# Optimization experiments

Measured on AMD Instinct MI355X. Metric: run time of the kernel, lower is better.

The kernel has to match this reference:

```python
import jax, jax.numpy as jnp
from jax import lax
import numpy as np

EMBED, HIDDEN, VOCAB = 512, 512, 10000
ATT, ENC = 512, 2048
B, NPIX, T = 128, 49, 30


def _lin(k, out_d, in_d):
    k1, k2 = jax.random.split(k)
    s = 1.0 / np.sqrt(in_d)
    return (jax.random.uniform(k1, (out_d, in_d), minval=-s, maxval=s),
            jax.random.uniform(k2, (out_d,), minval=-s, maxval=s))


def setup_inputs() -> dict:
    key = jax.random.key(0)
    ks = jax.random.split(key, 24)
    inp = {}
    inp['enc_image'] = jax.random.normal(ks[0], (B, NPIX, ENC))
    inp['global_features'] = jax.random.normal(ks[1], (B, ENC))
    inp['encoded_captions'] = jax.random.randint(ks[2], (B, T), 0, VOCAB)
    lens = jax.random.randint(ks[3], (B,), 1, T + 1).at[0].set(T)
    inp['caption_lengths'] = lens[:, None]
    # parameters
    inp['emb_W'] = jax.random.uniform(ks[4], (VOCAB, EMBED), minval=-0.1, maxval=0.1)
    inp['e2h_W'], inp['e2h_b'] = _lin(ks[5], HIDDEN, ENC)
    inp['gf_W'], inp['gf_b'] = _lin(ks[6], EMBED, ENC)
    inp['fc_W'] = jax.random.uniform(ks[7], (VOCAB, HIDDEN), minval=-0.1, maxval=0.1)
    inp['fc_b'] = jnp.zeros((VOCAB,))
    inp['lstm_Wih'], inp['lstm_bih'] = _lin(ks[8], 4 * HIDDEN, 2 * EMBED)
    inp['lstm_Whh'], inp['lstm_bhh'] = _lin(ks[9], 4 * HIDDEN, HIDDEN)
    inp['xg_W'], inp['xg_b'] = _lin(ks[10], HIDDEN, 2 * EMBED)
    inp['hg_W'], inp['hg_b'] = _lin(ks[11], HIDDEN, HIDDEN)
    inp['senaff_W'], inp['senaff_b'] = _lin(ks[12], HIDDEN, HIDDEN)
    inp['senatt_W'], inp['senatt_b'] = _lin(ks[13], ATT, HIDDEN)
    inp['haff_W'], inp['haff_b'] = _lin(ks[14], HIDDEN, HIDDEN)
    inp['hatt_W'], inp['hatt_b'] = _lin(ks[15], ATT, HIDDEN)
    inp['vatt_W'], inp['vatt_b'] = _lin(ks[16], ATT, HIDDEN)
    inp['alph_W'], inp['alph_b'] = _lin(ks[17], 1, ATT)
    inp['ctx_W'], inp['ctx_b'] = _lin(ks[18], HIDDEN, HIDDEN)
    return inp


def reference(enc_image, global_features, encoded_captions, caption_lengths,
              emb_W, e2h_W, e2h_b, gf_W, gf_b, fc_W, fc_b,
              lstm_Wih, lstm_bih, lstm_Whh, lstm_bhh,
              xg_W, xg_b, hg_W, hg_b,
              senaff_W, senaff_b, senatt_W, senatt_b,
              haff_W, haff_b, hatt_W, hatt_b,
              vatt_W, vatt_b, alph_W, alph_b, ctx_W, ctx_b):
    lengths = caption_lengths[:, 0]
    order = jnp.argsort(-lengths)                     # descending (stable)
    lengths = lengths[order]
    spatial = jax.nn.relu(jnp.einsum('bpe,he->bph', enc_image[order], e2h_W) + e2h_b)  # (B,NP,H)
    gimg = jax.nn.relu(global_features[order] @ gf_W.T + gf_b)                          # (B,E)
    embs = emb_W[encoded_captions[order]]                                               # (B,T,E)
    inputs = jnp.concatenate([embs, jnp.broadcast_to(gimg[:, None, :], embs.shape)], axis=-1)  # (B,T,2E)
    vattn = jnp.einsum('bph,ah->bpa', spatial, vatt_W) + vatt_b                         # (B,NP,A) hoisted
    h0 = jnp.zeros((spatial.shape[0], HIDDEN), spatial.dtype)
    c0 = h0

    def step(carry, xs):
        h, c = carry
        xt, mask = xs                                  # (B,2E), (B,) bool = row still active
        gates = xt @ lstm_Wih.T + lstm_bih + h @ lstm_Whh.T + lstm_bhh
        i, f, g, o = jnp.split(gates, 4, axis=-1)
        c_new = jax.nn.sigmoid(f) * c + jax.nn.sigmoid(i) * jnp.tanh(g)
        h_new = jax.nn.sigmoid(o) * jnp.tanh(c_new)
        st = jax.nn.sigmoid(xt @ xg_W.T + xg_b + h @ hg_W.T + hg_b) * jnp.tanh(c_new)  # sentinel
        sen_aff = jax.nn.relu(st @ senaff_W.T + senaff_b)    # (B,H)
        sen_att = sen_aff @ senatt_W.T + senatt_b            # (B,A)
        h_aff = jnp.tanh(h_new @ haff_W.T + haff_b)
        h_att = h_aff @ hatt_W.T + hatt_b
        att_feats = jnp.concatenate([vattn, sen_att[:, None, :]], axis=1)   # (B,NP+1,A)
        scores = jnp.tanh(att_feats + h_att[:, None, :]) @ alph_W[0] + alph_b[0]
        alpha = jax.nn.softmax(scores, axis=1)               # (B,NP+1)
        cat_feats = jnp.concatenate([spatial, sen_aff[:, None, :]], axis=1)
        context = jnp.einsum('bph,bp->bh', cat_feats, alpha)
        out_l = jnp.tanh((context + h_aff) @ ctx_W.T + ctx_b)
        pt = out_l @ fc_W.T + fc_b                           # dropout = identity (eval)
        m = mask[:, None]
        return (jnp.where(m, h_new, h), jnp.where(m, c_new, c)), jnp.where(m, pt, 0.0)

    masks = lengths[None, :] > jnp.arange(T)[:, None]        # (T,B) replicates shrinking batch_size_t
    _, preds = lax.scan(step, (h0, c0), (jnp.swapaxes(inputs, 0, 1), masks))
    return jnp.swapaxes(preds, 0, 1)                         # (B,T,VOCAB), sorted-by-length order
```

## Files before the change

kernel.cpp:

```cpp
#include <hip/hip_runtime.h>
#include <hip/hip_bf16.h>
#include <cstdint>
#include <cstddef>

#define DEVI __device__ __forceinline__

#define BB 128
#define TT 30
#define VOCAB 10000
#define ENCD 2048
#define NPIX 49
#define SLOT 65536

typedef __attribute__((ext_vector_type(8))) short bf16x8;
typedef __attribute__((ext_vector_type(4))) float f32x4;

DEVI float bf2f(unsigned short u){ union{float f; unsigned int i;} x; x.i=((unsigned)u)<<16; return x.f; }
DEVI unsigned short f2bf(float f){ union{float f; unsigned int i;} x; x.f=f; unsigned r=x.i + 0x7fffu + ((x.i>>16)&1u); return (unsigned short)(r>>16); }
DEVI float sigm(float x){ return 1.0f/(1.0f+expf(-x)); }
DEVI f32x4 mfma16(bf16x8 a, bf16x8 b, f32x4 c){ return __builtin_amdgcn_mfma_f32_16x16x32_bf16(a,b,c,0,0,0); }

DEVI uint4 byp16(const void* p){
  const unsigned long long* q=(const unsigned long long*)p;
  unsigned long long a=__hip_atomic_load(q,   __ATOMIC_RELAXED, __HIP_MEMORY_SCOPE_AGENT);
  unsigned long long b=__hip_atomic_load(q+1, __ATOMIC_RELAXED, __HIP_MEMORY_SCOPE_AGENT);
  uint4 r; r.x=(unsigned)a; r.y=(unsigned)(a>>32); r.z=(unsigned)b; r.w=(unsigned)(b>>32); return r;
}
DEVI unsigned byp4(const void* p){
  return __hip_atomic_load((const unsigned*)p, __ATOMIC_RELAXED, __HIP_MEMORY_SCOPE_AGENT);
}
DEVI void byps4(unsigned short* p, unsigned v){
  __hip_atomic_store((unsigned*)p, v, __ATOMIC_RELAXED, __HIP_MEMORY_SCOPE_AGENT);
}

DEVI void waitarr(int* base, int n, int thresh){
  __syncthreads();
  if(threadIdx.x < 64){
    for(;;){
      int v = (threadIdx.x<n) ? __hip_atomic_load(base + threadIdx.x*16, __ATOMIC_RELAXED, __HIP_MEMORY_SCOPE_AGENT)
                              : 0x7fffffff;
      if(__all(v >= thresh)) break;
      __builtin_amdgcn_s_sleep(8);
    }
  }
  asm volatile("" ::: "memory");
  __syncthreads();
}
DEVI void setflag(int* f, int val){
  __syncthreads();
  if(threadIdx.x==0) __hip_atomic_store(f, val, __ATOMIC_RELAXED, __HIP_MEMORY_SCOPE_AGENT);
}

__global__ void k_sort(const int* __restrict__ lens, int* __restrict__ order, int* __restrict__ Bt){
  __shared__ int L[BB];
  int i = threadIdx.x;
  L[i] = lens[i];
  __syncthreads();
  int li = L[i]; int rank = 0;
  for(int j=0;j<BB;j++){ int lj=L[j]; rank += (lj>li) || (lj==li && j<i); }
  order[rank] = i;
  if(i<TT){ int c=0; for(int j=0;j<BB;j++) c += (L[j]>i); Bt[i]=c; }
}

struct WC13 { const float* src[13]; unsigned short* dst[13]; int n[13]; };
__global__ void k_wconv(WC13 wc){
  int stride = gridDim.x*blockDim.x;
  int tid0 = blockIdx.x*blockDim.x + threadIdx.x;
  for(int s=0;s<13;s++){
    const float4* src=(const float4*)wc.src[s];
    int n4 = wc.n[s]>>2;
    ushort4* dst=(ushort4*)wc.dst[s];
    for(int i=tid0;i<n4;i+=stride){
      float4 v=src[i];
      ushort4 o; o.x=f2bf(v.x); o.y=f2bf(v.y); o.z=f2bf(v.z); o.w=f2bf(v.w);
      dst[i]=o;
    }
  }
}

__global__ void k_xt(const int* __restrict__ caps, const int* __restrict__ order,
                     const float* __restrict__ embW, const unsigned short* __restrict__ gimg,
                     unsigned short* __restrict__ xt){
  int total=BB*TT*1024;
  for(int idx=blockIdx.x*blockDim.x+threadIdx.x; idx<total; idx+=gridDim.x*blockDim.x){
    int k=idx&1023; int bt=idx>>10; int t=bt%TT; int b=bt/TT;
    unsigned short v;
    if(k<512){ int tok=caps[order[b]*TT+t]; v=f2bf(embW[(size_t)tok*512+k]); }
    else v=gimg[b*512+(k-512)];
    xt[idx]=v;
  }
}

__global__ __launch_bounds__(256) void k_gemm_f32A2(
    const float* __restrict__ A, int lda, int rpb, const int* __restrict__ order,
    const unsigned short* __restrict__ W, const float* __restrict__ bias,
    unsigned short* __restrict__ out, int K)
{
  __shared__ unsigned short As[128][136];
  int tid=threadIdx.x, wave=tid>>6, lane=tid&63, l15=lane&15, l4=lane>>4;
  int mb = blockIdx.y*128;
  f32x4 acc[8][4];
  f32x4 z = {0.f,0.f,0.f,0.f};
  #pragma unroll
  for(int i=0;i<8;i++)
    #pragma unroll
    for(int j=0;j<4;j++) acc[i][j]=z;
  int cch=tid&15, r0=tid>>4;
  int nb = blockIdx.x*256 + wave*64;
  for(int kc=0;kc<K;kc+=128){
    __syncthreads();
    #pragma unroll
    for(int rp=0;rp<8;rp++){
      int r=r0+rp*16;
      int m=mb+r;
      int sb = order[m/rpb]*rpb + m%rpb;
      const float* p = A + (size_t)sb*lda + kc + cch*8;
      float4 v0=*(const float4*)p, v1=*(const float4*)(p+4);
      unsigned short* d=&As[r][cch*8];
      d[0]=f2bf(v0.x); d[1]=f2bf(v0.y); d[2]=f2bf(v0.z); d[3]=f2bf(v0.w);
      d[4]=f2bf(v1.x); d[5]=f2bf(v1.y); d[6]=f2bf(v1.z); d[7]=f2bf(v1.w);
    }
    __syncthreads();
    #pragma unroll
    for(int kk=0;kk<4;kk++){
      bf16x8 bfr[4];
      #pragma unroll
      for(int nt=0;nt<4;nt++)
        bfr[nt] = *(const bf16x8*)(W + (size_t)(nb+nt*16+l15)*K + kc + kk*32 + l4*8);
      #pragma unroll
      for(int mt=0;mt<8;mt++){
        bf16x8 af = *(const bf16x8*)&As[mt*16+l15][kk*32+l4*8];
        #pragma unroll
        for(int nt=0;nt<4;nt++) acc[mt][nt]=mfma16(af,bfr[nt],acc[mt][nt]);
      }
    }
  }
  #pragma unroll
  for(int nt=0;nt<4;nt++){
    int n = nb + nt*16 + l15;
    float bs = bias[n];
    #pragma unroll
    for(int mt=0;mt<8;mt++){
      #pragma unroll
      for(int j=0;j<4;j++){
        int row = mb + mt*16 + l4*4 + j;
        float v = acc[mt][nt][j]+bs; v = v>0.f ? v : 0.f;
        out[(size_t)row*512 + n] = f2bf(v);
      }
    }
  }
}

DEVI void dev_gemm512c(unsigned short (*As)[136], const unsigned short* A, const unsigned short* W,
                       const float* bias, unsigned short* out, int xtile){
  int tid=threadIdx.x, wave=tid>>6, lane=tid&63, l15=lane&15, l4=lane>>4;
  f32x4 acc[8];
  f32x4 z = {0.f,0.f,0.f,0.f};
  #pragma unroll
  for(int i=0;i<8;i++) acc[i]=z;
  int cch=tid&15, r0=tid>>4;
  int nrow = xtile*64 + wave*16 + l15;
  for(int kc=0;kc<512;kc+=128){
    __syncthreads();
    #pragma unroll
    for(int rp=0;rp<8;rp++){
      int r=r0+rp*16;
      *(uint4*)&As[r][cch*8] = *(const uint4*)(A + (size_t)r*512 + kc + cch*8);
    }
    __syncthreads();
    #pragma unroll
    for(int kk=0;kk<4;kk++){
      bf16x8 bfr = *(const bf16x8*)(W + (size_t)nrow*512 + kc + kk*32 + l4*8);
      #pragma unroll
      for(int mt=0;mt<8;mt++){
        bf16x8 af = *(const bf16x8*)&As[mt*16+l15][kk*32+l4*8];
        acc[mt]=mfma16(af,bfr,acc[mt]);
      }
    }
  }
  float bs = bias ? bias[nrow] : 0.f;
  #pragma unroll
  for(int mt=0;mt<8;mt++){
    #pragma unroll
    for(int j=0;j<4;j++){
      int row = mt*16 + l4*4 + j;
      out[(size_t)row*512+nrow]=f2bf(acc[mt][j]+bs);
    }
  }
  __syncthreads();
}

struct PreD { const unsigned short* A; const unsigned short* W; const float* bias; unsigned short* out; };
struct PreD2 { PreD d[2]; };
__global__ __launch_bounds__(256) void k_pre(PreD2 dd){
  __shared__ unsigned short As[128][136];
  PreD g = dd.d[blockIdx.z];
  dev_gemm512c(As, g.A + (size_t)blockIdx.y*128*512, g.W, g.bias,
               g.out + (size_t)blockIdx.y*128*512, blockIdx.x);
}

__global__ __launch_bounds__(256) void k_gx(
    const unsigned short* __restrict__ xt, const unsigned short* __restrict__ w_ih,
    const unsigned short* __restrict__ w_xg,
    const float* __restrict__ bih, const float* __restrict__ bhh,
    const float* __restrict__ bxg, const float* __restrict__ bhg,
    unsigned short* __restrict__ Gx)
{
  __shared__ unsigned short As[128][136];
  int tid=threadIdx.x, wave=tid>>6, lane=tid&63, l15=lane&15, l4=lane>>4;
  int t = blockIdx.y;
  f32x4 acc[8];
  f32x4 z = {0.f,0.f,0.f,0.f};
  #pragma unroll
  for(int i=0;i<8;i++) acc[i]=z;
  int cch=tid&15, r0=tid>>4;
  int n = blockIdx.x*64 + wave*16 + l15;
  const unsigned short* wrow = (n<2048) ? (w_ih + (size_t)n*1024) : (w_xg + (size_t)(n-2048)*1024);
  for(int kc=0;kc<1024;kc+=128){
    __syncthreads();
    #pragma unroll
    for(int rp=0;rp<8;rp++){
      int r=r0+rp*16;
      *(uint4*)&As[r][cch*8] = *(const uint4*)(xt + (size_t)r*(TT*1024) + t*1024 + kc + cch*8);
    }
    __syncthreads();
    #pragma unroll
    for(int kk=0;kk<4;kk++){
      bf16x8 bfr = *(const bf16x8*)(wrow + kc + kk*32 + l4*8);
      #pragma unroll
      for(int mt=0;mt<8;mt++){
        bf16x8 af = *(const bf16x8*)&As[mt*16+l15][kk*32+l4*8];
        acc[mt]=mfma16(af,bfr,acc[mt]);
      }
    }
  }
  float bias = (n<2048) ? (bih[n]+bhh[n]) : (bxg[n-2048]+bhg[n-2048]);
  #pragma unroll
  for(int mt=0;mt<8;mt++){
    int row = mt*16 + l4*4;
    ushort4 o;
    o.x=f2bf(acc[mt][0]+bias); o.y=f2bf(acc[mt][1]+bias);
    o.z=f2bf(acc[mt][2]+bias); o.w=f2bf(acc[mt][3]+bias);
    *(ushort4*)(Gx + ((size_t)t*2560 + n)*128 + row) = o;
  }
}

struct PCtx {
  const unsigned short *w_hh, *w_hg, *Gx;
  const unsigned short *w_saff, *w_satt, *w_haff, *w_hatt, *w_ctx, *w_fc;
  const unsigned short *vattn, *SC;
  const float *sab,*stbias,*hab,*htb, *alW,*alb, *cxb, *fcb;
  const int *Bt;
  unsigned short *h_hist;
  unsigned short *stb;
  unsigned short *sbuf;
  float *dout;
  int *Lf,*SAf,*SBf,*S3f;
};

DEVI void stage_full(unsigned short (*As2)[520], const unsigned short* src){
  int tid=threadIdx.x;
  #pragma unroll
  for(int i=0;i<32;i++){
    int idx = i*256 + tid;
    int r = idx>>6, c = (idx&63)<<3;
    *(uint4*)&As2[r][c] = byp16(src + (size_t)r*512 + c);
  }
}

DEVI void dev_lstm3(unsigned short (*As2)[520], const PCtx& p, int t, int cb,
                    const unsigned short* hprev, unsigned short* hout, float creg[2][4]){
  int tid=threadIdx.x, wave=tid>>6, lane=tid&63, l15=lane&15, l4=lane>>4;
  int jb = cb*16;
  __syncthreads();
  stage_full(As2, hprev);
  f32x4 acc[2][5];
  #pragma unroll
  for(int m=0;m<2;m++){
    #pragma unroll
    for(int s=0;s<5;s++){
      int col = (s<4) ? (s*512 + jb + l15) : (2048 + jb + l15);
      int row = (wave*2+m)*16 + l4*4;
      ushort4 g = *(const ushort4*)(p.Gx + ((size_t)t*2560 + col)*128 + row);
      acc[m][s][0]=bf2f(g.x); acc[m][s][1]=bf2f(g.y); acc[m][s][2]=bf2f(g.z); acc[m][s][3]=bf2f(g.w);
    }
  }
  __syncthreads();
  #pragma unroll
  for(int kk=0;kk<16;kk++){
    int kg = kk*32 + l4*8;
    bf16x8 bfr[5];
    #pragma unroll
    for(int s=0;s<5;s++){
      const unsigned short* wp = (s<4) ? (p.w_hh + (size_t)(s*512+jb+l15)*512 + kg)
                                       : (p.w_hg + (size_t)(jb+l15)*512 + kg);
      bfr[s] = *(const bf16x8*)wp;
    }
    #pragma unroll
    for(int m=0;m<2;m++){
      bf16x8 af = *(const bf16x8*)&As2[(wave*2+m)*16+l15][kk*32+l4*8];
      #pragma unroll
      for(int s=0;s<5;s++) acc[m][s]=mfma16(af,bfr[s],acc[m][s]);
    }
  }
  int bt = p.Bt[t];
  int j = jb + l15;
  unsigned short* stt = p.stb + (size_t)t*SLOT;
  #pragma unroll
  for(int m=0;m<2;m++){
    int mt = wave*2+m;
    #pragma unroll
    for(int jj=0;jj<4;jj++){
      int b = mt*16 + l4*4 + jj;
      float iv = sigm(acc[m][0][jj]);
      float fv = sigm(acc[m][1][jj]);
      float gv = tanhf(acc[m][2][jj]);
      float ov = sigm(acc[m][3][jj]);
      float sv = sigm(acc[m][4][jj]);
      float cn = fv*creg[m][jj] + iv*gv;
      float tc = tanhf(cn);
      int hw = f2bf(ov*tc);
      int sw = f2bf(sv*tc);
      int hp = __shfl_xor(hw,1);
      int sp = __shfl_xor(sw,1);
      if((l15&1)==0){
        unsigned hword;
        if(b<bt) hword = (unsigned)(hw&0xffff) | ((unsigned)hp<<16);
        else     hword = byp4(hprev + (size_t)b*512 + j);
        byps4(hout + (size_t)b*512 + j, hword);
        byps4(stt  + (size_t)b*512 + j, (unsigned)(sw&0xffff) | ((unsigned)sp<<16));
      }
      if(b<bt) creg[m][jj]=cn;
    }
  }
}

DEVI void dev_mmA(unsigned short (*As2)[520], const unsigned short* Asrc, const unsigned short* W,
                  const float* bias, unsigned short* out, int act, int xtile){
  int tid=threadIdx.x, wave=tid>>6, lane=tid&63, l15=lane&15, l4=lane>>4;
  __syncthreads();
  stage_full(As2, Asrc);
  __syncthreads();
  f32x4 acc[8];
  f32x4 z = {0.f,0.f,0.f,0.f};
  #pragma unroll
  for(int i=0;i<8;i++) acc[i]=z;
  int nrow = xtile*64 + wave*16 + l15;
  #pragma unroll
  for(int kk=0;kk<16;kk++){
    bf16x8 bfr = *(const bf16x8*)(W + (size_t)nrow*512 + kk*32 + l4*8);
    #pragma unroll
    for(int mt=0;mt<8;mt++){
      bf16x8 af = *(const bf16x8*)&As2[mt*16+l15][kk*32+l4*8];
      acc[mt]=mfma16(af,bfr,acc[mt]);
    }
  }
  float bs = bias ? bias[nrow] : 0.f;
  #pragma unroll
  for(int mt=0;mt<8;mt++){
    #pragma unroll
    for(int j=0;j<4;j++){
      float v = acc[mt][j]+bs;
      if(act==1) v = fmaxf(v,0.f);
      else if(act==2) v = tanhf(v);
      int w = f2bf(v);
      int pw = __shfl_xor(w,1);
      if((l15&1)==0){
        int row = mt*16 + l4*4 + j;
        byps4(out + (size_t)row*512 + (nrow&~1), (unsigned)(w&0xffff) | ((unsigned)pw<<16));
      }
    }
  }
}

DEVI void dev_attn(float* sS, float* sA, unsigned short* sHA, unsigned short* sSA,
                   int b, const PCtx& p,
                   const unsigned short* satt, const unsigned short* hatt,
                   const unsigned short* scs, const unsigned short* sch,
                   unsigned short* outl){
  int tid=threadIdx.x;
  if(tid<64)       *(uint4*)&sHA[tid*8] = byp16(hatt + (size_t)b*512 + tid*8);
  else if(tid<128){ int q=tid-64; *(uint4*)&sSA[q*8] = byp16(satt + (size_t)b*512 + q*8); }
  __syncthreads();
  int gid=tid>>4, gl=tid&15;
  #pragma unroll
  for(int rp=0;rp<4;rp++){
    int pp = rp*16 + gid;
    float s = 0.f;
    if(pp<50){
      if(pp<NPIX){
        const unsigned short* vp = p.vattn + ((size_t)b*NPIX + pp)*512;
        #pragma unroll 8
        for(int k=gl*32;k<gl*32+32;k++) s += tanhf(bf2f(vp[k]) + bf2f(sHA[k])) * p.alW[k];
      } else {
        #pragma unroll 8
        for(int k=gl*32;k<gl*32+32;k++) s += tanhf(bf2f(sSA[k]) + bf2f(sHA[k])) * p.alW[k];
      }
    }
    #pragma unroll
    for(int off=8;off>=1;off>>=1) s += __shfl_xor(s, off);
    if(gl==0 && pp<50) sS[pp] = s + p.alb[0];
  }
  __syncthreads();
  if(tid<64){
    float sv = (tid<50) ? sS[tid] : -1e30f;
    float m = sv;
    #pragma unroll
    for(int off=32;off>=1;off>>=1) m = fmaxf(m, __shfl_xor(m, off));
    float e = (tid<50) ? expf(sv-m) : 0.f;
    float sum = e;
    #pragma unroll
    for(int off=32;off>=1;off>>=1) sum += __shfl_xor(sum, off);
    if(tid<50) sA[tid] = e/sum;
  }
  __syncthreads();
  float a49 = sA[49];
  {
    int n0 = tid*2;
    unsigned schU = byp4(sch + (size_t)b*512 + n0);
    unsigned scsU = byp4(scs + (size_t)b*512 + n0);
    float c0 = bf2f((unsigned short)schU), c1 = bf2f((unsigned short)(schU>>16));
    float s0 = bf2f((unsigned short)scsU), s1 = bf2f((unsigned short)(scsU>>16));
    float acc0 = c0 + a49*s0 + p.cxb[n0];
    float acc1 = c1 + a49*s1 + p.cxb[n0+1];
    const unsigned short* sp = p.SC + (size_t)b*NPIX*512 + n0;
    #pragma unroll 7
    for(int pp=0;pp<NPIX;pp++){
      unsigned u = *(const unsigned*)(sp + (size_t)pp*512);
      acc0 += sA[pp]*bf2f((unsigned short)u);
      acc1 += sA[pp]*bf2f((unsigned short)(u>>16));
    }
    unsigned o = ((unsigned)f2bf(tanhf(acc1))<<16) | (unsigned)(f2bf(tanhf(acc0))&0xffff);
    byps4(outl + (size_t)b*512 + n0, o);
  }
  __syncthreads();
}

DEVI void dev_fc2(unsigned short (*As2)[520], const PCtx& p, int t, int f,
                  const unsigned short* outl){
  int tid=threadIdx.x;
  __syncthreads();
  stage_full(As2, outl);
  __syncthreads();
  int wave=tid>>6, lane=tid&63, l15=lane&15, l4=lane>>4;
  int bt = p.Bt[t];
  for(int x=f; x<157; x+=112){
    f32x4 acc[8];
    f32x4 z = {0.f,0.f,0.f,0.f};
    #pragma unroll
    for(int i=0;i<8;i++) acc[i]=z;
    int nbase = x*64 + wave*16;
    int nr = nbase + l15; if(nr > VOCAB-1) nr = VOCAB-1;
    #pragma unroll 4
    for(int kk=0;kk<16;kk++){
      bf16x8 bfr = *(const bf16x8*)(p.w_fc + (size_t)nr*512 + kk*32 + l4*8);
      #pragma unroll
      for(int mt=0;mt<8;mt++){
        if(mt*16 < bt){
          bf16x8 af = *(const bf16x8*)&As2[mt*16+l15][kk*32+l4*8];
          acc[mt]=mfma16(af,bfr,acc[mt]);
        }
      }
    }
    int n = nbase + l15; bool nok = n < VOCAB;
    float bs = nok ? p.fcb[n] : 0.f;
    #pragma unroll
    for(int mt=0;mt<8;mt++){
      #pragma unroll
      for(int j=0;j<4;j++){
        int b = mt*16 + l4*4 + j;
        float v = (b<bt) ? (acc[mt][j]+bs) : 0.f;
        if(nok) p.dout[(size_t)b*(TT*VOCAB) + (size_t)t*VOCAB + n] = v;
      }
    }
  }
}

__global__ __launch_bounds__(256) void k_persist(PCtx p){
  __shared__ __align__(16) char smem[133760];
  auto As2 = (unsigned short (*)[520])smem;
  unsigned short* sHA = (unsigned short*)smem;
  unsigned short* sSA = sHA + 512;
  float* sS = (float*)(smem + 2048);
  float* sA = sS + 64;
  int cb = blockIdx.x;

  if(cb < 32){
    float creg[2][4];
    #pragma unroll
    for(int m=0;m<2;m++)
      #pragma unroll
      for(int j=0;j<4;j++) creg[m][j]=0.f;
    for(int t=0;t<TT;t++){
      if(t>0) waitarr(p.Lf, 32, t);
      dev_lstm3(As2, p, t, cb, p.h_hist + (size_t)t*SLOT, p.h_hist + (size_t)(t+1)*SLOT, creg);
      setflag(p.Lf + cb*16, t+1);
    }
  } else if(cb < 48){
    int w = cb-32;
    for(int t=0;t<TT;t++){
      waitarr(p.Lf, 32, t+1);
      unsigned short* S = p.sbuf + (size_t)t*7*SLOT;
      if(w<8) dev_mmA(As2, p.stb + (size_t)t*SLOT,          p.w_saff, p.sab, S,      1, w);
      else    dev_mmA(As2, p.h_hist + (size_t)(t+1)*SLOT,   p.w_haff, p.hab, S+SLOT, 2, w-8);
      setflag(p.SAf + w*16, t+1);
    }
  } else if(cb < 80){
    int w = cb-48;
    for(int t=0;t<TT;t++){
      waitarr(p.SAf, 16, t+1);
      unsigned short* S = p.sbuf + (size_t)t*7*SLOT;
      if(w<8)       dev_mmA(As2, S,      p.w_satt, p.stbias, S+2*SLOT, 0, w);
      else if(w<16) dev_mmA(As2, S+SLOT, p.w_hatt, p.htb,    S+3*SLOT, 0, w-8);
      else if(w<24) dev_mmA(As2, S,      p.w_ctx,  nullptr,  S+4*SLOT, 0, w-16);
      else          dev_mmA(As2, S+SLOT, p.w_ctx,  nullptr,  S+5*SLOT, 0, w-24);
      setflag(p.SBf + w*16, t+1);
    }
  } else if(cb < 144){
    int w = cb-80;
    for(int t=0;t<TT;t++){
      waitarr(p.SBf, 32, t+1);
      unsigned short* S = p.sbuf + (size_t)t*7*SLOT;
      dev_attn(sS,sA,sHA,sSA, w*2,   p, S+2*SLOT, S+3*SLOT, S+4*SLOT, S+5*SLOT, S+6*SLOT);
      dev_attn(sS,sA,sHA,sSA, w*2+1, p, S+2*SLOT, S+3*SLOT, S+4*SLOT, S+5*SLOT, S+6*SLOT);
      setflag(p.S3f + w*16, t+1);
    }
  } else {
    int f = cb-144;
    for(int t=0;t<TT;t++){
      waitarr(p.S3f, 64, t+1);
      unsigned short* S = p.sbuf + (size_t)t*7*SLOT;
      dev_fc2(As2, p, t, f, S+6*SLOT);
    }
  }
}

extern "C" void kernel_launch(void* const* d_in, const int* in_sizes, int n_in,
                              void* d_out, int out_size, void* d_ws, size_t ws_size,
                              hipStream_t stream)
{
  const float* enc  =(const float*)d_in[0];
  const float* gfeat=(const float*)d_in[1];
  const int*   caps =(const int*)d_in[2];
  const int*   lens =(const int*)d_in[3];
  const float* embW =(const float*)d_in[4];
  const float* e2hW =(const float*)d_in[5];  const float* e2hb=(const float*)d_in[6];
  const float* gfW  =(const float*)d_in[7];  const float* gfb =(const float*)d_in[8];
  const float* fcW  =(const float*)d_in[9];  const float* fcb =(const float*)d_in[10];
  const float* WihF =(const float*)d_in[11]; const float* bih =(const float*)d_in[12];
  const float* WhhF =(const float*)d_in[13]; const float* bhh =(const float*)d_in[14];
  const float* xgWF =(const float*)d_in[15]; const float* bxg =(const float*)d_in[16];
  const float* hgWF =(const float*)d_in[17]; const float* bhg =(const float*)d_in[18];
  const float* saWF =(const float*)d_in[19]; const float* sab =(const float*)d_in[20];
  const float* stWF =(const float*)d_in[21]; const float* stbias=(const float*)d_in[22];
  const float* haWF =(const float*)d_in[23]; const float* hab =(const float*)d_in[24];
  const float* htWF =(const float*)d_in[25]; const float* htb =(const float*)d_in[26];
  const float* vaWF =(const float*)d_in[27]; const float* vab =(const float*)d_in[28];
  const float* alW  =(const float*)d_in[29]; const float* alb =(const float*)d_in[30];
  const float* cxWF =(const float*)d_in[31]; const float* cxb =(const float*)d_in[32];

  char* base=(char*)d_ws; size_t off=0;
  auto alloc=[&](size_t bytes)->void*{ void* r=base+off; off += (bytes+255)&~(size_t)255; return r; };

  int* order=(int*)alloc(BB*4);
  int* Bt   =(int*)alloc(32*4);
  unsigned short* w_e2h =(unsigned short*)alloc((size_t)512*2048*2);
  unsigned short* w_gf  =(unsigned short*)alloc((size_t)512*2048*2);
  unsigned short* w_fc  =(unsigned short*)alloc((size_t)VOCAB*512*2);
  unsigned short* w_ih  =(unsigned short*)alloc((size_t)2048*1024*2);
  unsigned short* w_hh  =(unsigned short*)alloc((size_t)2048*512*2);
  unsigned short* w_xg  =(unsigned short*)alloc((size_t)512*1024*2);
  unsigned short* w_hg  =(unsigned short*)alloc((size_t)512*512*2);
  unsigned short* w_saff=(unsigned short*)alloc((size_t)512*512*2);
  unsigned short* w_satt=(unsigned short*)alloc((size_t)512*512*2);
  unsigned short* w_haff=(unsigned short*)alloc((size_t)512*512*2);
  unsigned short* w_hatt=(unsigned short*)alloc((size_t)512*512*2);
  unsigned short* w_vatt=(unsigned short*)alloc((size_t)512*512*2);
  unsigned short* w_ctx =(unsigned short*)alloc((size_t)512*512*2);
  unsigned short* spatial=(unsigned short*)alloc((size_t)BB*NPIX*512*2);
  unsigned short* vattn  =(unsigned short*)alloc((size_t)BB*NPIX*512*2);
  unsigned short* SC     =(unsigned short*)alloc((size_t)BB*NPIX*512*2);
  unsigned short* gimg   =(unsigned short*)alloc((size_t)BB*512*2);
  unsigned short* xt     =(unsigned short*)alloc((size_t)BB*TT*1024*2);
  int* flags =(int*)alloc(16384);
  unsigned short* Gx  =(unsigned short*)alloc((size_t)TT*2560*128*2);
  unsigned short* sbuf=(unsigned short*)alloc((size_t)TT*7*SLOT*2);

  unsigned short* stb_hist = w_e2h;
  unsigned short* h_hist   = spatial;

  k_sort<<<1,BB,0,stream>>>(lens, order, Bt);

  WC13 wc;
  const float* srcs[13] = {e2hW,gfW,fcW,WihF,WhhF,xgWF,hgWF,saWF,stWF,haWF,htWF,vaWF,cxWF};
  unsigned short* dsts[13] = {w_e2h,w_gf,w_fc,w_ih,w_hh,w_xg,w_hg,w_saff,w_satt,w_haff,w_hatt,w_vatt,w_ctx};
  int ns[13] = {512*2048,512*2048,VOCAB*512,2048*1024,2048*512,512*1024,512*512,512*512,512*512,512*512,512*512,512*512,512*512};
  for(int i=0;i<13;i++){ wc.src[i]=srcs[i]; wc.dst[i]=dsts[i]; wc.n[i]=ns[i]; }
  k_wconv<<<1024,256,0,stream>>>(wc);

  k_gemm_f32A2<<<dim3(2,NPIX),256,0,stream>>>(enc, ENCD, NPIX, order, w_e2h, e2hb, spatial, ENCD);
  k_gemm_f32A2<<<dim3(2,1),  256,0,stream>>>(gfeat, ENCD, 1, order, w_gf, gfb, gimg, ENCD);
  k_xt<<<1024,256,0,stream>>>(caps, order, embW, gimg, xt);
  {
    PreD2 dv{};
    dv.d[0] = PreD{spatial, w_vatt, vab,     vattn};
    dv.d[1] = PreD{spatial, w_ctx,  nullptr, SC};
    k_pre<<<dim3(8,NPIX,2),256,0,stream>>>(dv);
  }
  k_gx<<<dim3(40,TT),256,0,stream>>>(xt, w_ih, w_xg, bih, bhh, bxg, bhg, Gx);

  hipMemsetAsync(h_hist, 0, (size_t)SLOT*2, stream);
  hipMemsetAsync(flags, 0, 16384, stream);

  PCtx pc;
  pc.w_hh=w_hh; pc.w_hg=w_hg; pc.Gx=Gx;
  pc.w_saff=w_saff; pc.w_satt=w_satt; pc.w_haff=w_haff; pc.w_hatt=w_hatt; pc.w_ctx=w_ctx; pc.w_fc=w_fc;
  pc.vattn=vattn; pc.SC=SC;
  pc.sab=sab; pc.stbias=stbias; pc.hab=hab; pc.htb=htb;
  pc.alW=alW; pc.alb=alb; pc.cxb=cxb; pc.fcb=fcb;
  pc.Bt=Bt;
  pc.h_hist=h_hist; pc.stb=stb_hist; pc.sbuf=sbuf;
  pc.dout=(float*)d_out;
  pc.Lf  = flags;
  pc.SAf = flags + 32*16;
  pc.SBf = flags + 48*16;
  pc.S3f = flags + 80*16;

  k_persist<<<256,256,0,stream>>>(pc);
}
```

Measured before the change: 2.780 ms.

## Shrink persistent kernel block count and skip inactive batch rows per step

The persistent pipeline drops from 256 to 120 blocks. Each LSTM block now handles two 16-column hidden tiles, and each mid-stage block computes two output tiles. Matmuls stage and multiply only the active batch rows (rounded up to 16), the t=0 recurrent matmul is skipped because the initial hidden state is zero, and attention work is skipped for finished captions. The aim is less flag-synchronisation fan-in and less wasted work on padded rows. The trade-off is that far fewer blocks now serve the vocabulary projection (16 instead of 112), so that stage may become the pipeline bottleneck.

Result: slower. 8.426 ms (+203.1%).

```diff
diff --git a/kernel.cpp b/kernel.cpp
--- a/kernel.cpp
+++ b/kernel.cpp
@@ -258,116 +258,128 @@
   int *Lf,*SAf,*SBf,*S3f;
 };
 
-DEVI void stage_full(unsigned short (*As2)[520], const unsigned short* src){
+DEVI void stage_rows(unsigned short (*As2)[520], const unsigned short* src, int mrows){
   int tid=threadIdx.x;
-  #pragma unroll
-  for(int i=0;i<32;i++){
+  int iters = mrows>>2;
+  for(int i=0;i<iters;i++){
     int idx = i*256 + tid;
     int r = idx>>6, c = (idx&63)<<3;
     *(uint4*)&As2[r][c] = byp16(src + (size_t)r*512 + c);
   }
 }
 
-DEVI void dev_lstm3(unsigned short (*As2)[520], const PCtx& p, int t, int cb,
-                    const unsigned short* hprev, unsigned short* hout, float creg[2][4]){
+DEVI void dev_lstmM(unsigned short (*As2)[520], const PCtx& p, int t, int cb,
+                    const unsigned short* hprev, unsigned short* hout, float creg[2][2][4]){
   int tid=threadIdx.x, wave=tid>>6, lane=tid&63, l15=lane&15, l4=lane>>4;
-  int jb = cb*16;
-  __syncthreads();
-  stage_full(As2, hprev);
-  f32x4 acc[2][5];
-  #pragma unroll
-  for(int m=0;m<2;m++){
-    #pragma unroll
-    for(int s=0;s<5;s++){
-      int col = (s<4) ? (s*512 + jb + l15) : (2048 + jb + l15);
-      int row = (wave*2+m)*16 + l4*4;
-      ushort4 g = *(const ushort4*)(p.Gx + ((size_t)t*2560 + col)*128 + row);
-      acc[m][s][0]=bf2f(g.x); acc[m][s][1]=bf2f(g.y); acc[m][s][2]=bf2f(g.z); acc[m][s][3]=bf2f(g.w);
-    }
-  }
-  __syncthreads();
-  #pragma unroll
-  for(int kk=0;kk<16;kk++){
-    int kg = kk*32 + l4*8;
-    bf16x8 bfr[5];
-    #pragma unroll
-    for(int s=0;s<5;s++){
-      const unsigned short* wp = (s<4) ? (p.w_hh + (size_t)(s*512+jb+l15)*512 + kg)
-                                       : (p.w_hg + (size_t)(jb+l15)*512 + kg);
-      bfr[s] = *(const bf16x8*)wp;
-    }
+  int bt = p.Bt[t];
+  int mrows = (bt+15)&~15, mtiles = mrows>>4;
+  __syncthreads();
+  if(t>0) stage_rows(As2, hprev, mrows);
+  __syncthreads();
+  unsigned short* stt = p.stb + (size_t)t*SLOT;
+  #pragma unroll
+  for(int nt=0;nt<2;nt++){
+    int jb = cb*32 + nt*16;
+    f32x4 acc[2][5];
     #pragma unroll
     for(int m=0;m<2;m++){
-      bf16x8 af = *(const bf16x8*)&As2[(wave*2+m)*16+l15][kk*32+l4*8];
-      #pragma unroll
-      for(int s=0;s<5;s++) acc[m][s]=mfma16(af,bfr[s],acc[m][s]);
-    }
-  }
-  int bt = p.Bt[t];
-  int j = jb + l15;
-  unsigned short* stt = p.stb + (size_t)t*SLOT;
-  #pragma unroll
-  for(int m=0;m<2;m++){
-    int mt = wave*2+m;
-    #pragma unroll
-    for(int jj=0;jj<4;jj++){
-      int b = mt*16 + l4*4 + jj;
-      float iv = sigm(acc[m][0][jj]);
-      float fv = sigm(acc[m][1][jj]);
-      float gv = tanhf(acc[m][2][jj]);
-      float ov = sigm(acc[m][3][jj]);
-      float sv = sigm(acc[m][4][jj]);
-      float cn = fv*creg[m][jj] + iv*gv;
-      float tc = tanhf(cn);
-      int hw = f2bf(ov*tc);
-      int sw = f2bf(sv*tc);
-      int hp = __shfl_xor(hw,1);
-      int sp = __shfl_xor(sw,1);
-      if((l15&1)==0){
-        unsigned hword;
-        if(b<bt) hword = (unsigned)(hw&0xffff) | ((unsigned)hp<<16);
-        else     hword = byp4(hprev + (size_t)b*512 + j);
-        byps4(hout + (size_t)b*512 + j, hword);
-        byps4(stt  + (size_t)b*512 + j, (unsigned)(sw&0xffff) | ((unsigned)sp<<16));
-      }
-      if(b<bt) creg[m][jj]=cn;
-    }
-  }
-}
-
-DEVI void dev_mmA(unsigned short (*As2)[520], const unsigned short* Asrc, const unsigned short* W,
-                  const float* bias, unsigned short* out, int act, int xtile){
+      #pragma unroll
+      for(int s=0;s<5;s++){
+        int col = (s<4) ? (s*512 + jb + l15) : (2048 + jb + l15);
+        int row = (wave*2+m)*16 + l4*4;
+        ushort4 g = *(const ushort4*)(p.Gx + ((size_t)t*2560 + col)*128 + row);
+        acc[m][s][0]=bf2f(g.x); acc[m][s][1]=bf2f(g.y); acc[m][s][2]=bf2f(g.z); acc[m][s][3]=bf2f(g.w);
+      }
+    }
+    if(t>0){
+      #pragma unroll
+      for(int kk=0;kk<16;kk++){
+        int kg = kk*32 + l4*8;
+        bf16x8 bfr[5];
+        #pragma unroll
+        for(int s=0;s<5;s++){
+          const unsigned short* wp = (s<4) ? (p.w_hh + (size_t)(s*512+jb+l15)*512 + kg)
+                                           : (p.w_hg + (size_t)(jb+l15)*512 + kg);
+          bfr[s] = *(const bf16x8*)wp;
+        }
+        #pragma unroll
+        for(int m=0;m<2;m++){
+          int mt = wave*2+m;
+          if(mt < mtiles){
+            bf16x8 af = *(const bf16x8*)&As2[mt*16+l15][kk*32+l4*8];
+            #pragma unroll
+            for(int s=0;s<5;s++) acc[m][s]=mfma16(af,bfr[s],acc[m][s]);
+          }
+        }
+      }
+    }
+    int j = jb + l15;
+    #pragma unroll
+    for(int m=0;m<2;m++){
+      int mt = wave*2+m;
+      #pragma unroll
+      for(int jj=0;jj<4;jj++){
+        int b = mt*16 + l4*4 + jj;
+        float iv = sigm(acc[m][0][jj]);
+        float fv = sigm(acc[m][1][jj]);
+        float gv = tanhf(acc[m][2][jj]);
+        float ov = sigm(acc[m][3][jj]);
+        float sv = sigm(acc[m][4][jj]);
+        float cn = fv*creg[nt][m][jj] + iv*gv;
+        float tc = tanhf(cn);
+        int hw = f2bf(ov*tc);
+        int sw = f2bf(sv*tc);
+        int hp = __shfl_xor(hw,1);
+        int sp = __shfl_xor(sw,1);
+        if(b<bt){
+          if((l15&1)==0){
+            byps4(hout + (size_t)b*512 + j, (unsigned)(hw&0xffff) | ((unsigned)hp<<16));
+            byps4(stt  + (size_t)b*512 + j, (unsigned)(sw&0xffff) | ((unsigned)sp<<16));
+          }
+          creg[nt][m][jj]=cn;
+        }
+      }
+    }
+  }
+}
+
+DEVI void dev_mm2(unsigned short (*As2)[520], const unsigned short* src, const unsigned short* W,
+                  const float* bias, unsigned short* out, int act, int x0, int bt){
   int tid=threadIdx.x, wave=tid>>6, lane=tid&63, l15=lane&15, l4=lane>>4;
-  __syncthreads();
-  stage_full(As2, Asrc);
-  __syncthreads();
-  f32x4 acc[8];
-  f32x4 z = {0.f,0.f,0.f,0.f};
-  #pragma unroll
-  for(int i=0;i<8;i++) acc[i]=z;
-  int nrow = xtile*64 + wave*16 + l15;
-  #pragma unroll
-  for(int kk=0;kk<16;kk++){
-    bf16x8 bfr = *(const bf16x8*)(W + (size_t)nrow*512 + kk*32 + l4*8);
+  int mrows = (bt+15)&~15, mtiles = mrows>>4;
+  __syncthreads();
+  stage_rows(As2, src, mrows);
+  __syncthreads();
+  for(int xi=0;xi<2;xi++){
+    int nrow = (x0+xi)*64 + wave*16 + l15;
+    f32x4 acc[8];
+    f32x4 z = {0.f,0.f,0.f,0.f};
+    #pragma unroll
+    for(int i=0;i<8;i++) acc[i]=z;
+    #pragma unroll
+    for(int kk=0;kk<16;kk++){
+      bf16x8 bfr = *(const bf16x8*)(W + (size_t)nrow*512 + kk*32 + l4*8);
+      #pragma unroll
+      for(int mt=0;mt<8;mt++){
+        if(mt < mtiles){
+          bf16x8 af = *(const bf16x8*)&As2[mt*16+l15][kk*32+l4*8];
+          acc[mt]=mfma16(af,bfr,acc[mt]);
+        }
+      }
+    }
+    float bs = bias ? bias[nrow] : 0.f;
     #pragma unroll
     for(int mt=0;mt<8;mt++){
-      bf16x8 af = *(const bf16x8*)&As2[mt*16+l15][kk*32+l4*8];
-      acc[mt]=mfma16(af,bfr,acc[mt]);
-    }
-  }
-  float bs = bias ? bias[nrow] : 0.f;
-  #pragma unroll
-  for(int mt=0;mt<8;mt++){
-    #pragma unroll
-    for(int j=0;j<4;j++){
-      float v = acc[mt][j]+bs;
-      if(act==1) v = fmaxf(v,0.f);
-      else if(act==2) v = tanhf(v);
-      int w = f2bf(v);
-      int pw = __shfl_xor(w,1);
-      if((l15&1)==0){
+      #pragma unroll
+      for(int j=0;j<4;j++){
+        float v = acc[mt][j]+bs;
+        if(act==1) v = fmaxf(v,0.f);
+        else if(act==2) v = tanhf(v);
+        int w = f2bf(v);
+        int pw = __shfl_xor(w,1);
         int row = mt*16 + l4*4 + j;
-        byps4(out + (size_t)row*512 + (nrow&~1), (unsigned)(w&0xffff) | ((unsigned)pw<<16));
+        if((l15&1)==0 && row<bt)
+          byps4(out + (size_t)row*512 + (nrow&~1), (unsigned)(w&0xffff) | ((unsigned)pw<<16));
       }
     }
   }
@@ -436,15 +448,16 @@
   __syncthreads();
 }
 
-DEVI void dev_fc2(unsigned short (*As2)[520], const PCtx& p, int t, int f,
+DEVI void dev_fcM(unsigned short (*As2)[520], const PCtx& p, int t, int f,
                   const unsigned short* outl){
   int tid=threadIdx.x;
-  __syncthreads();
-  stage_full(As2, outl);
+  int bt = p.Bt[t];
+  int mrows = (bt+15)&~15, mtiles = mrows>>4;
+  __syncthreads();
+  stage_rows(As2, outl, mrows);
   __syncthreads();
   int wave=tid>>6, lane=tid&63, l15=lane&15, l4=lane>>4;
-  int bt = p.Bt[t];
-  for(int x=f; x<157; x+=112){
+  for(int x=f; x<157; x+=16){
     f32x4 acc[8];
     f32x4 z = {0.f,0.f,0.f,0.f};
     #pragma unroll
@@ -456,7 +469,7 @@
       bf16x8 bfr = *(const bf16x8*)(p.w_fc + (size_t)nr*512 + kk*32 + l4*8);
       #pragma unroll
       for(int mt=0;mt<8;mt++){
-        if(mt*16 < bt){
+        if(mt < mtiles){
           bf16x8 af = *(const bf16x8*)&As2[mt*16+l15][kk*32+l4*8];
           acc[mt]=mfma16(af,bfr,acc[mt]);
         }
@@ -485,52 +498,62 @@
   float* sA = sS + 64;
   int cb = blockIdx.x;
 
-  if(cb < 32){
-    float creg[2][4];
-    #pragma unroll
-    for(int m=0;m<2;m++)
-      #pragma unroll
-      for(int j=0;j<4;j++) creg[m][j]=0.f;
+  if(cb < 16){
+    float creg[2][2][4];
+    #pragma unroll
+    for(int a=0;a<2;a++)
+      #pragma unroll
+      for(int m=0;m<2;m++)
+        #pragma unroll
+        for(int j=0;j<4;j++) creg[a][m][j]=0.f;
     for(int t=0;t<TT;t++){
-      if(t>0) waitarr(p.Lf, 32, t);
-      dev_lstm3(As2, p, t, cb, p.h_hist + (size_t)t*SLOT, p.h_hist + (size_t)(t+1)*SLOT, creg);
+      if(t>0) waitarr(p.Lf, 16, t);
+      dev_lstmM(As2, p, t, cb, p.h_hist + (size_t)t*SLOT, p.h_hist + (size_t)(t+1)*SLOT, creg);
       setflag(p.Lf + cb*16, t+1);
     }
-  } else if(cb < 48){
-    int w = cb-32;
+  } else if(cb < 24){
+    int w = cb-16;
     for(int t=0;t<TT;t++){
-      waitarr(p.Lf, 32, t+1);
+      waitarr(p.Lf, 16, t+1);
+      int bt = p.Bt[t];
       unsigned short* S = p.sbuf + (size_t)t*7*SLOT;
-      if(w<8) dev_mmA(As2, p.stb + (size_t)t*SLOT,          p.w_saff, p.sab, S,      1, w);
-      else    dev_mmA(As2, p.h_hist + (size_t)(t+1)*SLOT,   p.w_haff, p.hab, S+SLOT, 2, w-8);
+      if(w<4) dev_mm2(As2, p.stb + (size_t)t*SLOT,        p.w_saff, p.sab, S,      1, w*2,     bt);
+      else    dev_mm2(As2, p.h_hist + (size_t)(t+1)*SLOT, p.w_haff, p.hab, S+SLOT, 2, (w-4)*2, bt);
       setflag(p.SAf + w*16, t+1);
     }
-  } else if(cb < 80){
-    int w = cb-48;
+  } else if(cb < 40){
+    int w = cb-24;
+    int q = w>>2, x0 = (w&3)*2;
     for(int t=0;t<TT;t++){
-      waitarr(p.SAf, 16, t+1);
+      waitarr(p.SAf, 8, t+1);
+      int bt = p.Bt[t];
       unsigned short* S = p.sbuf + (size_t)t*7*SLOT;
-      if(w<8)       dev_mmA(As2, S,      p.w_satt, p.stbias, S+2*SLOT, 0, w);
-      else if(w<16) dev_mmA(As2, S+SLOT, p.w_hatt, p.htb,    S+3*SLOT, 0, w-8);
-      else if(w<24) dev_mmA(As2, S,      p.w_ctx,  nullptr,  S+4*SLOT, 0, w-16);
-      else          dev_mmA(As2, S+SLOT, p.w_ctx,  nullptr,  S+5*SLOT, 0, w-24);
+      const unsigned short* src = (q==0||q==2) ? S : S+SLOT;
+      const unsigned short* W   = (q==0)? p.w_satt : (q==1)? p.w_hatt : p.w_ctx;
+      const float* bias         = (q==0)? p.stbias : (q==1)? p.htb    : nullptr;
+      unsigned short* out       = S + (size_t)(2+q)*SLOT;
+      dev_mm2(As2, src, W, bias, out, 0, x0, bt);
       setflag(p.SBf + w*16, t+1);
     }
-  } else if(cb < 144){
-    int w = cb-80;
+  } else if(cb < 104){
+    int w = cb-40;
     for(int t=0;t<TT;t++){
-      waitarr(p.SBf, 32, t+1);
+      waitarr(p.SBf, 16, t+1);
+      int bt = p.Bt[t];
       unsigned short* S = p.sbuf + (size_t)t*7*SLOT;
-      dev_attn(sS,sA,sHA,sSA, w*2,   p, S+2*SLOT, S+3*SLOT, S+4*SLOT, S+5*SLOT, S+6*SLOT);
-      dev_attn(sS,sA,sHA,sSA, w*2+1, p, S+2*SLOT, S+3*SLOT, S+4*SLOT, S+5*SLOT, S+6*SLOT);
+      #pragma unroll
+      for(int r=0;r<2;r++){
+        int b = w*2+r;
+        if(b < bt) dev_attn(sS,sA,sHA,sSA, b, p, S+2*SLOT, S+3*SLOT, S+4*SLOT, S+5*SLOT, S+6*SLOT);
+      }
       setflag(p.S3f + w*16, t+1);
     }
   } else {
-    int f = cb-144;
+    int f = cb-104;
     for(int t=0;t<TT;t++){
       waitarr(p.S3f, 64, t+1);
       unsigned short* S = p.sbuf + (size_t)t*7*SLOT;
-      dev_fc2(As2, p, t, f, S+6*SLOT);
+      dev_fcM(As2, p, t, f, S+6*SLOT);
     }
   }
 }
@@ -622,9 +645,9 @@
   pc.h_hist=h_hist; pc.stb=stb_hist; pc.sbuf=sbuf;
   pc.dout=(float*)d_out;
   pc.Lf  = flags;
-  pc.SAf = flags + 32*16;
-  pc.SBf = flags + 48*16;
-  pc.S3f = flags + 80*16;
-
-  k_persist<<<256,256,0,stream>>>(pc);
-}
+  pc.SAf = flags + 256;
+  pc.SBf = flags + 384;
+  pc.S3f = flags + 640;
+
+  k_persist<<<120,256,0,stream>>>(pc);
+}
```

## Skip finished batch rows and use plain cached loads in persistent decoder

Applied to the files above, without the earlier changes.

The persistent decoder now skips the recurrent matmul at t=0, skips attention for batch rows whose caption has ended, and stops writing outputs for rows at or beyond the active batch size. Relaxed agent-scope atomic loads and stores are replaced with ordinary vector loads and stores, and the flag store becomes a release store. The h and sentinel history buffers get their own allocations instead of aliasing weight and feature buffers, so the initial memset is dropped. The aim is less wasted work on padded rows and cheaper memory accesses, at the risk of reading stale cross-workgroup data through non-coherent caches, since the readers do not use acquire loads.

Result: no change. 2.803 ms (+0.8%).

```diff
diff --git a/kernel.cpp b/kernel.cpp
--- a/kernel.cpp
+++ b/kernel.cpp
@@ -20,19 +20,6 @@
 DEVI float sigm(float x){ return 1.0f/(1.0f+expf(-x)); }
 DEVI f32x4 mfma16(bf16x8 a, bf16x8 b, f32x4 c){ return __builtin_amdgcn_mfma_f32_16x16x32_bf16(a,b,c,0,0,0); }
 
-DEVI uint4 byp16(const void* p){
-  const unsigned long long* q=(const unsigned long long*)p;
-  unsigned long long a=__hip_atomic_load(q,   __ATOMIC_RELAXED, __HIP_MEMORY_SCOPE_AGENT);
-  unsigned long long b=__hip_atomic_load(q+1, __ATOMIC_RELAXED, __HIP_MEMORY_SCOPE_AGENT);
-  uint4 r; r.x=(unsigned)a; r.y=(unsigned)(a>>32); r.z=(unsigned)b; r.w=(unsigned)(b>>32); return r;
-}
-DEVI unsigned byp4(const void* p){
-  return __hip_atomic_load((const unsigned*)p, __ATOMIC_RELAXED, __HIP_MEMORY_SCOPE_AGENT);
-}
-DEVI void byps4(unsigned short* p, unsigned v){
-  __hip_atomic_store((unsigned*)p, v, __ATOMIC_RELAXED, __HIP_MEMORY_SCOPE_AGENT);
-}
-
 DEVI void waitarr(int* base, int n, int thresh){
   __syncthreads();
   if(threadIdx.x < 64){
@@ -48,7 +35,7 @@
 }
 DEVI void setflag(int* f, int val){
   __syncthreads();
-  if(threadIdx.x==0) __hip_atomic_store(f, val, __ATOMIC_RELAXED, __HIP_MEMORY_SCOPE_AGENT);
+  if(threadIdx.x==0) __hip_atomic_store(f, val, __ATOMIC_RELEASE, __HIP_MEMORY_SCOPE_AGENT);
 }
 
 __global__ void k_sort(const int* __restrict__ lens, int* __restrict__ order, int* __restrict__ Bt){
@@ -264,16 +251,17 @@
   for(int i=0;i<32;i++){
     int idx = i*256 + tid;
     int r = idx>>6, c = (idx&63)<<3;
-    *(uint4*)&As2[r][c] = byp16(src + (size_t)r*512 + c);
-  }
-}
-
-DEVI void dev_lstm3(unsigned short (*As2)[520], const PCtx& p, int t, int cb,
+    *(uint4*)&As2[r][c] = *(const uint4*)(src + (size_t)r*512 + c);
+  }
+}
+
+DEVI void dev_lstmP(unsigned short (*As2)[520], const PCtx& p, int t, int cb,
                     const unsigned short* hprev, unsigned short* hout, float creg[2][4]){
   int tid=threadIdx.x, wave=tid>>6, lane=tid&63, l15=lane&15, l4=lane>>4;
   int jb = cb*16;
-  __syncthreads();
-  stage_full(As2, hprev);
+  int bt = p.Bt[t];
+  __syncthreads();
+  if(t>0) stage_full(As2, hprev);
   f32x4 acc[2][5];
   #pragma unroll
   for(int m=0;m<2;m++){
@@ -286,24 +274,25 @@
     }
   }
   __syncthreads();
-  #pragma unroll
-  for(int kk=0;kk<16;kk++){
-    int kg = kk*32 + l4*8;
-    bf16x8 bfr[5];
-    #pragma unroll
-    for(int s=0;s<5;s++){
-      const unsigned short* wp = (s<4) ? (p.w_hh + (size_t)(s*512+jb+l15)*512 + kg)
-                                       : (p.w_hg + (size_t)(jb+l15)*512 + kg);
-      bfr[s] = *(const bf16x8*)wp;
-    }
-    #pragma unroll
-    for(int m=0;m<2;m++){
-      bf16x8 af = *(const bf16x8*)&As2[(wave*2+m)*16+l15][kk*32+l4*8];
-      #pragma unroll
-      for(int s=0;s<5;s++) acc[m][s]=mfma16(af,bfr[s],acc[m][s]);
-    }
-  }
-  int bt = p.Bt[t];
+  if(t>0){
+    #pragma unroll
+    for(int kk=0;kk<16;kk++){
+      int kg = kk*32 + l4*8;
+      bf16x8 bfr[5];
+      #pragma unroll
+      for(int s=0;s<5;s++){
+        const unsigned short* wp = (s<4) ? (p.w_hh + (size_t)(s*512+jb+l15)*512 + kg)
+                                         : (p.w_hg + (size_t)(jb+l15)*512 + kg);
+        bfr[s] = *(const bf16x8*)wp;
+      }
+      #pragma unroll
+      for(int m=0;m<2;m++){
+        bf16x8 af = *(const bf16x8*)&As2[(wave*2+m)*16+l15][kk*32+l4*8];
+        #pragma unroll
+        for(int s=0;s<5;s++) acc[m][s]=mfma16(af,bfr[s],acc[m][s]);
+      }
+    }
+  }
   int j = jb + l15;
   unsigned short* stt = p.stb + (size_t)t*SLOT;
   #pragma unroll
@@ -323,29 +312,28 @@
       int sw = f2bf(sv*tc);
       int hp = __shfl_xor(hw,1);
       int sp = __shfl_xor(sw,1);
-      if((l15&1)==0){
-        unsigned hword;
-        if(b<bt) hword = (unsigned)(hw&0xffff) | ((unsigned)hp<<16);
-        else     hword = byp4(hprev + (size_t)b*512 + j);
-        byps4(hout + (size_t)b*512 + j, hword);
-        byps4(stt  + (size_t)b*512 + j, (unsigned)(sw&0xffff) | ((unsigned)sp<<16));
-      }
-      if(b<bt) creg[m][jj]=cn;
-    }
-  }
-}
-
-DEVI void dev_mmA(unsigned short (*As2)[520], const unsigned short* Asrc, const unsigned short* W,
-                  const float* bias, unsigned short* out, int act, int xtile){
+      if(b<bt){
+        if((l15&1)==0){
+          *(unsigned*)(hout + (size_t)b*512 + j) = (unsigned)(hw&0xffff) | ((unsigned)hp<<16);
+          *(unsigned*)(stt  + (size_t)b*512 + j) = (unsigned)(sw&0xffff) | ((unsigned)sp<<16);
+        }
+        creg[m][jj]=cn;
+      }
+    }
+  }
+}
+
+DEVI void dev_mm1(unsigned short (*As2)[520], const unsigned short* src, const unsigned short* W,
+                  const float* bias, unsigned short* out, int act, int xtile, int bt){
   int tid=threadIdx.x, wave=tid>>6, lane=tid&63, l15=lane&15, l4=lane>>4;
   __syncthreads();
-  stage_full(As2, Asrc);
-  __syncthreads();
+  stage_full(As2, src);
+  __syncthreads();
+  int nrow = xtile*64 + wave*16 + l15;
   f32x4 acc[8];
   f32x4 z = {0.f,0.f,0.f,0.f};
   #pragma unroll
   for(int i=0;i<8;i++) acc[i]=z;
-  int nrow = xtile*64 + wave*16 + l15;
   #pragma unroll
   for(int kk=0;kk<16;kk++){
     bf16x8 bfr = *(const bf16x8*)(W + (size_t)nrow*512 + kk*32 + l4*8);
@@ -365,10 +353,9 @@
       else if(act==2) v = tanhf(v);
       int w = f2bf(v);
       int pw = __shfl_xor(w,1);
-      if((l15&1)==0){
-        int row = mt*16 + l4*4 + j;
-        byps4(out + (size_t)row*512 + (nrow&~1), (unsigned)(w&0xffff) | ((unsigned)pw<<16));
-      }
+      int row = mt*16 + l4*4 + j;
+      if((l15&1)==0 && row<bt)
+        *(unsigned*)(out + (size_t)row*512 + (nrow&~1)) = (unsigned)(w&0xffff) | ((unsigned)pw<<16);
     }
   }
 }
@@ -379,8 +366,8 @@
                    const unsigned short* scs, const unsigned short* sch,
                    unsigned short* outl){
   int tid=threadIdx.x;
-  if(tid<64)       *(uint4*)&sHA[tid*8] = byp16(hatt + (size_t)b*512 + tid*8);
-  else if(tid<128){ int q=tid-64; *(uint4*)&sSA[q*8] = byp16(satt + (size_t)b*512 + q*8); }
+  if(tid<64)       *(uint4*)&sHA[tid*8] = *(const uint4*)(hatt + (size_t)b*512 + tid*8);
+  else if(tid<128){ int q=tid-64; *(uint4*)&sSA[q*8] = *(const uint4*)(satt + (size_t)b*512 + q*8); }
   __syncthreads();
   int gid=tid>>4, gl=tid&15;
   #pragma unroll
@@ -417,8 +404,8 @@
   float a49 = sA[49];
   {
     int n0 = tid*2;
-    unsigned schU = byp4(sch + (size_t)b*512 + n0);
-    unsigned scsU = byp4(scs + (size_t)b*512 + n0);
+    unsigned schU = *(const unsigned*)(sch + (size_t)b*512 + n0);
+    unsigned scsU = *(const unsigned*)(scs + (size_t)b*512 + n0);
     float c0 = bf2f((unsigned short)schU), c1 = bf2f((unsigned short)(schU>>16));
     float s0 = bf2f((unsigned short)scsU), s1 = bf2f((unsigned short)(scsU>>16));
     float acc0 = c0 + a49*s0 + p.cxb[n0];
@@ -431,19 +418,19 @@
       acc1 += sA[pp]*bf2f((unsigned short)(u>>16));
     }
     unsigned o = ((unsigned)f2bf(tanhf(acc1))<<16) | (unsigned)(f2bf(tanhf(acc0))&0xffff);
-    byps4(outl + (size_t)b*512 + n0, o);
-  }
-  __syncthreads();
-}
-
-DEVI void dev_fc2(unsigned short (*As2)[520], const PCtx& p, int t, int f,
+    *(unsigned*)(outl + (size_t)b*512 + n0) = o;
+  }
+  __syncthreads();
+}
+
+DEVI void dev_fcF(unsigned short (*As2)[520], const PCtx& p, int t, int f,
                   const unsigned short* outl){
   int tid=threadIdx.x;
+  int bt = p.Bt[t];
   __syncthreads();
   stage_full(As2, outl);
   __syncthreads();
   int wave=tid>>6, lane=tid&63, l15=lane&15, l4=lane>>4;
-  int bt = p.Bt[t];
   for(int x=f; x<157; x+=112){
     f32x4 acc[8];
     f32x4 z = {0.f,0.f,0.f,0.f};
@@ -493,36 +480,44 @@
       for(int j=0;j<4;j++) creg[m][j]=0.f;
     for(int t=0;t<TT;t++){
       if(t>0) waitarr(p.Lf, 32, t);
-      dev_lstm3(As2, p, t, cb, p.h_hist + (size_t)t*SLOT, p.h_hist + (size_t)(t+1)*SLOT, creg);
+      dev_lstmP(As2, p, t, cb, p.h_hist + (size_t)t*SLOT, p.h_hist + (size_t)(t+1)*SLOT, creg);
       setflag(p.Lf + cb*16, t+1);
     }
   } else if(cb < 48){
     int w = cb-32;
     for(int t=0;t<TT;t++){
       waitarr(p.Lf, 32, t+1);
+      int bt = p.Bt[t];
       unsigned short* S = p.sbuf + (size_t)t*7*SLOT;
-      if(w<8) dev_mmA(As2, p.stb + (size_t)t*SLOT,          p.w_saff, p.sab, S,      1, w);
-      else    dev_mmA(As2, p.h_hist + (size_t)(t+1)*SLOT,   p.w_haff, p.hab, S+SLOT, 2, w-8);
+      if(w<8) dev_mm1(As2, p.stb + (size_t)t*SLOT,        p.w_saff, p.sab, S,      1, w,   bt);
+      else    dev_mm1(As2, p.h_hist + (size_t)(t+1)*SLOT, p.w_haff, p.hab, S+SLOT, 2, w-8, bt);
       setflag(p.SAf + w*16, t+1);
     }
   } else if(cb < 80){
     int w = cb-48;
+    int q = w>>3, x0 = w&7;
     for(int t=0;t<TT;t++){
       waitarr(p.SAf, 16, t+1);
+      int bt = p.Bt[t];
       unsigned short* S = p.sbuf + (size_t)t*7*SLOT;
-      if(w<8)       dev_mmA(As2, S,      p.w_satt, p.stbias, S+2*SLOT, 0, w);
-      else if(w<16) dev_mmA(As2, S+SLOT, p.w_hatt, p.htb,    S+3*SLOT, 0, w-8);
-      else if(w<24) dev_mmA(As2, S,      p.w_ctx,  nullptr,  S+4*SLOT, 0, w-16);
-      else          dev_mmA(As2, S+SLOT, p.w_ctx,  nullptr,  S+5*SLOT, 0, w-24);
+      const unsigned short* src = (q==0||q==2) ? S : S+SLOT;
+      const unsigned short* W   = (q==0)? p.w_satt : (q==1)? p.w_hatt : p.w_ctx;
+      const float* bias         = (q==0)? p.stbias : (q==1)? p.htb    : nullptr;
+      unsigned short* out       = S + (size_t)(2+q)*SLOT;
+      dev_mm1(As2, src, W, bias, out, 0, x0, bt);
       setflag(p.SBf + w*16, t+1);
     }
   } else if(cb < 144){
     int w = cb-80;
     for(int t=0;t<TT;t++){
       waitarr(p.SBf, 32, t+1);
+      int bt = p.Bt[t];
       unsigned short* S = p.sbuf + (size_t)t*7*SLOT;
-      dev_attn(sS,sA,sHA,sSA, w*2,   p, S+2*SLOT, S+3*SLOT, S+4*SLOT, S+5*SLOT, S+6*SLOT);
-      dev_attn(sS,sA,sHA,sSA, w*2+1, p, S+2*SLOT, S+3*SLOT, S+4*SLOT, S+5*SLOT, S+6*SLOT);
+      #pragma unroll
+      for(int r=0;r<2;r++){
+        int b = w*2+r;
+        if(b < bt) dev_attn(sS,sA,sHA,sSA, b, p, S+2*SLOT, S+3*SLOT, S+4*SLOT, S+5*SLOT, S+6*SLOT);
+      }
       setflag(p.S3f + w*16, t+1);
     }
   } else {
@@ -530,7 +525,7 @@
     for(int t=0;t<TT;t++){
       waitarr(p.S3f, 64, t+1);
       unsigned short* S = p.sbuf + (size_t)t*7*SLOT;
-      dev_fc2(As2, p, t, f, S+6*SLOT);
+      dev_fcF(As2, p, t, f, S+6*SLOT);
     }
   }
 }
@@ -585,9 +580,8 @@
   int* flags =(int*)alloc(16384);
   unsigned short* Gx  =(unsigned short*)alloc((size_t)TT*2560*128*2);
   unsigned short* sbuf=(unsigned short*)alloc((size_t)TT*7*SLOT*2);
-
-  unsigned short* stb_hist = w_e2h;
-  unsigned short* h_hist   = spatial;
+  unsigned short* h_hist=(unsigned short*)alloc((size_t)(TT+1)*SLOT*2);
+  unsigned short* stb_hist=(unsigned short*)alloc((size_t)TT*SLOT*2);
 
   k_sort<<<1,BB,0,stream>>>(lens, order, Bt);
 
@@ -609,7 +603,6 @@
   }
   k_gx<<<dim3(40,TT),256,0,stream>>>(xt, w_ih, w_xg, bih, bhh, bxg, bhg, Gx);
 
-  hipMemsetAsync(h_hist, 0, (size_t)SLOT*2, stream);
   hipMemsetAsync(flags, 0, 16384, stream);
 
   PCtx pc;
```
